# Performance work log

Measured on AMD Instinct MI355X. Metric: run time of the kernel, lower is better.

Reference implementation:

```python
import jax, jax.numpy as jnp
import numpy as np

N_NODES = 50000
N_EDGES = 800000
IN_FEATS = 128
HIDDEN = 128
OUT_LEN = 128


def setup_inputs() -> dict:
    key = jax.random.key(0)
    ks = jax.random.split(key, 8)
    feat = jax.random.normal(ks[0], (N_NODES, IN_FEATS), dtype=jnp.float32)
    # Glorot-ish init for weights, zeros for bias (DGL GraphConv default)
    def w(k, fi, fo):
        return jax.random.normal(k, (fi, fo), dtype=jnp.float32) / np.sqrt(fi)
    W1 = w(ks[1], IN_FEATS, HIDDEN)
    W2 = w(ks[2], HIDDEN, HIDDEN)
    W3 = w(ks[3], HIDDEN, OUT_LEN)
    b1 = jnp.zeros((HIDDEN,), jnp.float32)
    b2 = jnp.zeros((HIDDEN,), jnp.float32)
    b3 = jnp.zeros((OUT_LEN,), jnp.float32)
    src = jax.random.randint(ks[4], (N_EDGES,), 0, N_NODES, dtype=jnp.int32)
    dst = jax.random.randint(ks[5], (N_EDGES,), 0, N_NODES, dtype=jnp.int32)
    return {"feat": feat, "W1": W1, "b1": b1, "W2": W2, "b2": b2,
            "W3": W3, "b3": b3, "src": src, "dst": dst}


def _degree_norm(idx, n):
    # degree counts, clamped to min 1 (DGL behavior), then ^{-1/2}
    deg = jax.ops.segment_sum(jnp.ones_like(idx, dtype=jnp.float32), idx,
                              num_segments=n)
    return jax.lax.rsqrt(jnp.maximum(deg, 1.0))


def _graph_conv(x, W, b, src, dst, out_norm, in_norm):
    # DGL GraphConv, norm='both':
    # h = D_dst^{-1/2} * segsum_dst( D_src^{-1/2} * x[src] ) @ W + b
    h = x * out_norm[:, None]
    m = jax.ops.segment_sum(h[src], dst, num_segments=x.shape[0])  # [N, d]
    m = m * in_norm[:, None]
    return m @ W + b


def reference(feat, W1, b1, W2, b2, W3, b3, src, dst):
    out_norm = _degree_norm(src, feat.shape[0])  # out-degree norm (source)
    in_norm = _degree_norm(dst, feat.shape[0])   # in-degree norm (dest)
    h = jax.nn.relu(_graph_conv(feat, W1, b1, src, dst, out_norm, in_norm))
    h = jax.nn.relu(_graph_conv(h, W2, b2, src, dst, out_norm, in_norm))
    h = _graph_conv(h, W3, b3, src, dst, out_norm, in_norm)
    # single graph: mean_nodes == mean over all nodes, then squeeze -> [out_len]
    return jnp.mean(h, axis=0)
```

## Files before the change

### kernel.cpp

```cpp
#include <hip/hip_runtime.h>

#define N_NODES 50000
#define N_EDGES 800000
#define F 128
#define SCAN_NB 49
#define CH 64
#define EPC (N_EDGES / CH)
#define HALF 25000
#define QTR 12500
#define BSTRIDE 17
#define AGG_NB (N_NODES / 4)
#define GB ((N_NODES + 63) / 64)

typedef __bf16 bf16x8 __attribute__((ext_vector_type(8)));
typedef float  f32x4  __attribute__((ext_vector_type(4)));
typedef float  f32x2  __attribute__((ext_vector_type(2)));

__device__ inline unsigned short f2bf(float f) {
    unsigned u = __float_as_uint(f);
    u += 0x7FFF + ((u >> 16) & 1);
    return (unsigned short)(u >> 16);
}
__device__ inline unsigned packbf2(float a, float b) {
    return (unsigned)f2bf(a) | ((unsigned)f2bf(b) << 16);
}

__device__ inline void fp8x8_to_f32(uint2 u, float* f) {
    f32x2 v0 = __builtin_amdgcn_cvt_pk_f32_fp8(u.x, false);
    f32x2 v1 = __builtin_amdgcn_cvt_pk_f32_fp8(u.x, true);
    f32x2 v2 = __builtin_amdgcn_cvt_pk_f32_fp8(u.y, false);
    f32x2 v3 = __builtin_amdgcn_cvt_pk_f32_fp8(u.y, true);
    f[0] = v0.x; f[1] = v0.y; f[2] = v1.x; f[3] = v1.y;
    f[4] = v2.x; f[5] = v2.y; f[6] = v3.x; f[7] = v3.y;
}
__device__ inline unsigned f32x4_to_fp8(float a, float b, float c, float d) {
    unsigned r = __builtin_amdgcn_cvt_pk_fp8_f32(a, b, 0, false);
    r = __builtin_amdgcn_cvt_pk_fp8_f32(c, d, r, true);
    return r;
}

__global__ __launch_bounds__(1024) void hist_kernel(const int* __restrict__ src,
                                                    const int* __restrict__ dst,
                                                    unsigned char* __restrict__ Hs8,
                                                    unsigned char* __restrict__ Hd8,
                                                    int* __restrict__ bsump) {
    __shared__ unsigned hist[HALF / 4];
    int bx = blockIdx.x;
    int c = bx >> 2, t = bx & 1, h = (bx >> 1) & 1;
    const int* ids = t ? dst : src;
    unsigned char* H = t ? Hd8 : Hs8;
    int base = h * HALF;
    for (int j = threadIdx.x; j < HALF / 4; j += 1024) hist[j] = 0;
    __syncthreads();
    const int4* ids4 = (const int4*)(ids + c * EPC);
    for (int i = threadIdx.x; i < EPC / 4; i += 1024) {
        int4 v = ids4[i];
#pragma unroll
        for (int k = 0; k < 4; k++) {
            int id = ((k == 0) ? v.x : (k == 1) ? v.y : (k == 2) ? v.z : v.w) - base;
            if ((unsigned)id < (unsigned)HALF)
                atomicAdd(&hist[id >> 2], 1u << ((id & 3) * 8));
        }
    }
    __syncthreads();
    unsigned* Hw = (unsigned*)(H + (size_t)c * N_NODES + base);
    for (int j = threadIdx.x; j < HALF / 4; j += 1024) Hw[j] = hist[j];
    if (t) {
        int w = threadIdx.x >> 6, lane = threadIdx.x & 63;
        for (int r = w; r < SCAN_NB; r += 16) {
            int gi0 = max(r * 1024, base);
            int gi1 = min(r * 1024 + 1024, base + HALF);
            int s = 0;
            for (int li = gi0 - base + lane; li < gi1 - base; li += 64)
                s += (hist[li >> 2] >> ((li & 3) * 8)) & 255;
#pragma unroll
            for (int off = 32; off; off >>= 1) s += __shfl_down(s, off);
            if (lane == 0) bsump[(c * 2 + h) * SCAN_NB + r] = s;
        }
    }
}

__global__ __launch_bounds__(1024) void scanC_kernel(const unsigned char* __restrict__ Hs8,
                                                     const unsigned char* __restrict__ Hd8,
                                                     const int* __restrict__ bsump,
                                                     float* __restrict__ onorm,
                                                     float* __restrict__ inorm,
                                                     int* __restrict__ rowst,
                                                     unsigned char* __restrict__ P8) {
    __shared__ int wsum[16];
    __shared__ int tot[SCAN_NB];
    int t = threadIdx.x, lane = t & 63, w = t >> 6;
    int i = blockIdx.x * 1024 + t;
    if (t < SCAN_NB) {
        int s = 0;
        for (int p = 0; p < 2 * CH; p++) s += bsump[p * SCAN_NB + t];
        tot[t] = s;
    }
    int dd = 0;
    if (i < N_NODES) {
        int ds = 0, run = 0;
        for (int c = 0; c < CH; c++) {
            size_t o = (size_t)c * N_NODES + i;
            ds += Hs8[o];
            P8[o] = (unsigned char)run;
            run += Hd8[o];
        }
        dd = run;
        onorm[i] = rsqrtf(fmaxf((float)ds, 1.0f));
        inorm[i] = rsqrtf(fmaxf((float)dd, 1.0f));
    }
    int v = dd, incl = v;
#pragma unroll
    for (int off = 1; off < 64; off <<= 1) {
        int u = __shfl_up(incl, off);
        if (lane >= off) incl += u;
    }
    if (lane == 63) wsum[w] = incl;
    __syncthreads();
    if (t == 0) {
        int s = 0;
        for (int r = 0; r < (int)blockIdx.x; r++) s += tot[r];
#pragma unroll
        for (int k = 0; k < 16; k++) { int x = wsum[k]; wsum[k] = s; s += x; }
    }
    __syncthreads();
    incl += wsum[w];
    if (i < N_NODES) {
        rowst[i] = incl - v;
        if (i == N_NODES - 1) rowst[N_NODES] = incl;
    }
}

__global__ __launch_bounds__(1024) void tqsc_kernel(const int* __restrict__ src,
                                                    const int* __restrict__ dst,
                                                    const float* __restrict__ inorm,
                                                    float* __restrict__ Tq,
                                                    const int* __restrict__ rowst,
                                                    const unsigned char* __restrict__ P8,
                                                    int* __restrict__ esrc,
                                                    const float* __restrict__ feat,
                                                    const float* __restrict__ onorm,
                                                    uint2* __restrict__ xq,
                                                    const float* __restrict__ W1,
                                                    const float* __restrict__ W2,
                                                    unsigned short* __restrict__ Wt) {
    __shared__ float a[QTR];
    __shared__ int cur[QTR];
    int bx = blockIdx.x;
    int c = bx >> 2, q = bx & 3;
    int base = q * QTR;

    for (int j = threadIdx.x; j < QTR; j += 1024) {
        a[j] = 0.0f;
        cur[j] = rowst[base + j] + (int)P8[(size_t)c * N_NODES + base + j];
    }
    __syncthreads();

    const int4* src4 = (const int4*)(src + c * EPC);
    const int4* dst4 = (const int4*)(dst + c * EPC);
    for (int i = threadIdx.x; i < EPC / 4; i += 1024) {
        int4 s4 = src4[i], d4 = dst4[i];
#pragma unroll
        for (int k = 0; k < 4; k++) {
            int s = (k == 0) ? s4.x : (k == 1) ? s4.y : (k == 2) ? s4.z : s4.w;
            int d = (k == 0) ? d4.x : (k == 1) ? d4.y : (k == 2) ? d4.z : d4.w;
            int sq = s - base;
            if ((unsigned)sq < (unsigned)QTR)
                atomicAdd(&a[sq], inorm[d]);
            int dq = d - base;
            if ((unsigned)dq < (unsigned)QTR) {
                int pos = atomicAdd(&cur[dq], 1);
                esrc[pos] = s;
            }
        }
    }
    __syncthreads();
    for (int j = threadIdx.x; j < QTR; j += 1024)
        Tq[(size_t)c * N_NODES + base + j] = a[j];

    int T = gridDim.x * 1024;
    int id0 = bx * 1024 + threadIdx.x;
    for (int i = id0; i < N_NODES * F / 8; i += T) {
        float w = onorm[i >> 4];
        const float4* xv = (const float4*)feat;
        float4 v0 = xv[i * 2], v1 = xv[i * 2 + 1];
        uint2 o;
        o.x = f32x4_to_fp8(v0.x * w, v0.y * w, v0.z * w, v0.w * w);
        o.y = f32x4_to_fp8(v1.x * w, v1.y * w, v1.z * w, v1.w * w);
        xq[i] = o;
    }
    for (int i = id0; i < 2 * F * F; i += T) {
        int wi = i >> 14, rem = i & 16383;
        int n = rem >> 7, k = rem & 127;
        const float* W = wi ? W2 : W1;
        Wt[(size_t)wi * F * F + (size_t)n * F + k] = f2bf(W[k * F + n]);
    }
}

template <int QT>
__global__ __launch_bounds__(256) void agg_csr_kernel(const uint2* __restrict__ xq,
                                                      uint4* __restrict__ mb,
                                                      const int* __restrict__ rowst,
                                                      const int* __restrict__ esrc,
                                                      const float* __restrict__ inorm,
                                                      const float* __restrict__ Tq,
                                                      float* __restrict__ qt) {
    int w = threadIdx.x >> 6;
    int lane = threadIdx.x & 63;
    int g = lane >> 4, t = lane & 15;
    int row = blockIdx.x * 4 + w;
    int beg = __builtin_amdgcn_readfirstlane(rowst[row]);
    int end = __builtin_amdgcn_readfirstlane(rowst[row + 1]);
    float acc[8];
#pragma unroll
    for (int k = 0; k < 8; k++) acc[k] = 0.0f;

    for (int e = beg; e < end; e += 16) {
        int ea = min(e + g,      end - 1);
        int eb = min(e + 4 + g,  end - 1);
        int ec = min(e + 8 + g,  end - 1);
        int ed = min(e + 12 + g, end - 1);
        int sa = esrc[ea], sb = esrc[eb], sc = esrc[ec], sd = esrc[ed];
        uint2 ua = xq[(size_t)sa * 16 + t];
        uint2 ub = xq[(size_t)sb * 16 + t];
        uint2 uc = xq[(size_t)sc * 16 + t];
        uint2 ud = xq[(size_t)sd * 16 + t];
        float wa = (e + g      < end) ? 1.0f : 0.0f;
        float wb = (e + 4 + g  < end) ? 1.0f : 0.0f;
        float wc = (e + 8 + g  < end) ? 1.0f : 0.0f;
        float wd = (e + 12 + g < end) ? 1.0f : 0.0f;
        float fa[8], fb[8], fc[8], fd[8];
        fp8x8_to_f32(ua, fa); fp8x8_to_f32(ub, fb);
        fp8x8_to_f32(uc, fc); fp8x8_to_f32(ud, fd);
#pragma unroll
        for (int k = 0; k < 8; k++)
            acc[k] += fa[k] * wa + fb[k] * wb + fc[k] * wc + fd[k] * wd;
    }
#pragma unroll
    for (int k = 0; k < 8; k++) {
        acc[k] += __shfl_xor(acc[k], 16, 64);
        acc[k] += __shfl_xor(acc[k], 32, 64);
    }
    if (g == 0) {
        float inw = inorm[row];
        uint4 o;
        o.x = packbf2(acc[0] * inw, acc[1] * inw);
        o.y = packbf2(acc[2] * inw, acc[3] * inw);
        o.z = packbf2(acc[4] * inw, acc[5] * inw);
        o.w = packbf2(acc[6] * inw, acc[7] * inw);
        mb[(size_t)row * 16 + t] = o;
    }
    if (QT) {
        int i = blockIdx.x * 256 + threadIdx.x;
        if (i < N_NODES) {
            float s = 0.0f;
            for (int c = 0; c < CH; c++) s += Tq[(size_t)c * N_NODES + i];
            qt[i] = s;
        }
    }
}

template <int FINAL>
__global__ __launch_bounds__(256) void mfma_gemm_kernel(const unsigned short* __restrict__ A,
                                                        const unsigned short* __restrict__ Wt,
                                                        const float* __restrict__ bias,
                                                        const float* __restrict__ onorm,
                                                        unsigned char* __restrict__ Y8,
                                                        const float* __restrict__ qt,
                                                        float* __restrict__ part2) {
    __shared__ uint4 sB[F * BSTRIDE];
    __shared__ float sPf[4][F];
    int tid = threadIdx.x;
    int w = tid >> 6;
    int lane = tid & 63;
    int quad = lane >> 4, r16 = lane & 15;
    int row0 = blockIdx.x * 64 + w * 16;

    int arow = min(row0 + r16, N_NODES - 1);
    const uint4* Arow = (const uint4*)(A + (size_t)arow * F);
    uint4 a[4];
#pragma unroll
    for (int kk = 0; kk < 4; kk++) a[kk] = Arow[kk * 4 + quad];

    const uint4* G = (const uint4*)Wt;
    for (int j = tid; j < F * 16; j += 256)
        sB[(j >> 4) * BSTRIDE + (j & 15)] = G[j];

    f32x4 acc[8];
#pragma unroll
    for (int t = 0; t < 8; t++) acc[t] = (f32x4){0.f, 0.f, 0.f, 0.f};
    __syncthreads();

#pragma unroll
    for (int kk = 0; kk < 4; kk++) {
        bf16x8 av = __builtin_bit_cast(bf16x8, a[kk]);
#pragma unroll
        for (int t = 0; t < 8; t++) {
            bf16x8 bv = __builtin_bit_cast(bf16x8,
                sB[(t * 16 + r16) * BSTRIDE + kk * 4 + quad]);
            acc[t] = __builtin_amdgcn_mfma_f32_16x16x32_bf16(av, bv, acc[t], 0, 0, 0);
        }
    }

    float rw[4];
#pragma unroll
    for (int reg = 0; reg < 4; reg++) {
        int row = row0 + quad * 4 + reg;
        rw[reg] = (row < N_NODES) ? (FINAL ? qt[row] * onorm[row] : onorm[row]) : 0.0f;
    }

    if (!FINAL) {
#pragma unroll
        for (int t = 0; t < 8; t++) {
            int col = t * 16 + r16;
            float bb = bias[col];
#pragma unroll
            for (int reg = 0; reg < 4; reg++) {
                int row = row0 + quad * 4 + reg;
                if (row < N_NODES) {
                    float v = fmaxf(acc[t][reg] + bb, 0.0f) * rw[reg];
                    unsigned p = __builtin_amdgcn_cvt_pk_fp8_f32(v, v, 0, false);
                    Y8[(size_t)row * F + col] = (unsigned char)(p & 0xFF);
                }
            }
        }
    } else {
#pragma unroll
        for (int t = 0; t < 8; t++) {
            int col = t * 16 + r16;
            float bb = bias[col];
            float p = 0.0f;
#pragma unroll
            for (int reg = 0; reg < 4; reg++)
                p += fmaxf(acc[t][reg] + bb, 0.0f) * rw[reg];
            p += __shfl_xor(p, 16, 64);
            p += __shfl_xor(p, 32, 64);
            if (quad == 0) sPf[w][col] = p;
        }
        __syncthreads();
        if (tid < F)
            part2[(size_t)blockIdx.x * F + tid] =
                sPf[0][tid] + sPf[1][tid] + sPf[2][tid] + sPf[3][tid];
    }
}

__global__ __launch_bounds__(1024) void final_kernel(const float* __restrict__ part2,
                                                     const float* __restrict__ W3,
                                                     const float* __restrict__ b3,
                                                     float* __restrict__ out) {
    __shared__ float sc[8][F];
    int tid = threadIdx.x;
    int col = tid & 127, sl = tid >> 7;
    float acc = 0.0f;
    for (int b = sl; b < GB; b += 8) acc += part2[(size_t)b * F + col];
    sc[sl][col] = acc;
    __syncthreads();
    if (tid < F) {
        float s = 0.0f;
#pragma unroll
        for (int k = 0; k < 8; k++) s += sc[k][tid];
        sc[0][tid] = s * (1.0f / (float)N_NODES);
    }
    __syncthreads();
    if (tid < F) {
        float o = b3[tid];
        for (int k = 0; k < F; k++) o += sc[0][k] * W3[k * F + tid];
        out[tid] = o;
    }
}

extern "C" void kernel_launch(void* const* d_in, const int* in_sizes, int n_in,
                              void* d_out, int out_size, void* d_ws, size_t ws_size,
                              hipStream_t stream) {
    const float* feat = (const float*)d_in[0];
    const float* W1   = (const float*)d_in[1];
    const float* b1   = (const float*)d_in[2];
    const float* W2   = (const float*)d_in[3];
    const float* b2   = (const float*)d_in[4];
    const float* W3   = (const float*)d_in[5];
    const float* b3   = (const float*)d_in[6];
    const int*   src  = (const int*)d_in[7];
    const int*   dst  = (const int*)d_in[8];
    float* out = (float*)d_out;

    char* ws = (char*)d_ws;
    size_t off = 0;
    uint4* mb    = (uint4*)(ws + off); off += (size_t)N_NODES * F * 2;
    float* Tq    = (float*)(ws + off); off += (size_t)CH * N_NODES * 4;
    uint2* xq    = (uint2*)(ws + off); off += (size_t)N_NODES * F;
    uint2* hq    = (uint2*)(ws + off); off += (size_t)N_NODES * F;
    unsigned char* Hs8 = (unsigned char*)(ws + off); off += (size_t)CH * N_NODES;
    unsigned char* Hd8 = (unsigned char*)(ws + off); off += (size_t)CH * N_NODES;
    unsigned char* P8  = (unsigned char*)(ws + off); off += (size_t)CH * N_NODES;
    int*   esrc  = (int*)  (ws + off); off += (size_t)N_EDGES * 4;
    unsigned short* Wt = (unsigned short*)(ws + off); off += 2 * F * F * 2;
    float* part2 = (float*)(ws + off); off += (size_t)GB * F * 4;
    float* onorm = (float*)(ws + off); off += N_NODES * 4;
    float* inorm = (float*)(ws + off); off += N_NODES * 4;
    float* qt    = (float*)(ws + off); off += N_NODES * 4;
    int*   rowst = (int*)  (ws + off); off += (N_NODES + 1) * 4;
    int*   bsump = (int*)  (ws + off); off += 2 * CH * SCAN_NB * 4;

    hist_kernel<<<4 * CH, 1024, 0, stream>>>(src, dst, Hs8, Hd8, bsump);
    scanC_kernel<<<SCAN_NB, 1024, 0, stream>>>(Hs8, Hd8, bsump, onorm, inorm,
                                               rowst, P8);
    tqsc_kernel<<<4 * CH, 1024, 0, stream>>>(src, dst, inorm, Tq, rowst, P8,
                                             esrc, feat, onorm, xq, W1, W2, Wt);

    agg_csr_kernel<1><<<AGG_NB, 256, 0, stream>>>(xq, mb, rowst, esrc, inorm, Tq, qt);
    mfma_gemm_kernel<0><<<GB, 256, 0, stream>>>((const unsigned short*)mb, Wt, b1,
                                                onorm, (unsigned char*)hq, qt, part2);
    agg_csr_kernel<0><<<AGG_NB, 256, 0, stream>>>(hq, mb, rowst, esrc, inorm, Tq, qt);
    mfma_gemm_kernel<1><<<GB, 256, 0, stream>>>((const unsigned short*)mb, Wt + F * F,
                                                b2, onorm, (unsigned char*)hq, qt, part2);
    final_kernel<<<1, 1024, 0, stream>>>(part2, W3, b3, out);
}
```

Measured before the change: 212.4 us.

## Split histogram into quarters and widen degree scan to 196 small blocks

After: 224.1 us. 1.05x slower.

```diff
diff --git a/kernel.cpp b/kernel.cpp
--- a/kernel.cpp
+++ b/kernel.cpp
@@ -3,10 +3,9 @@
 #define N_NODES 50000
 #define N_EDGES 800000
 #define F 128
-#define SCAN_NB 49
+#define RNG 196
 #define CH 64
 #define EPC (N_EDGES / CH)
-#define HALF 25000
 #define QTR 12500
 #define BSTRIDE 17
 #define AGG_NB (N_NODES / 4)
@@ -44,13 +43,13 @@
                                                     unsigned char* __restrict__ Hs8,
                                                     unsigned char* __restrict__ Hd8,
                                                     int* __restrict__ bsump) {
-    __shared__ unsigned hist[HALF / 4];
+    __shared__ unsigned hist[QTR / 4];
     int bx = blockIdx.x;
-    int c = bx >> 2, t = bx & 1, h = (bx >> 1) & 1;
+    int c = bx >> 3, t = bx & 1, h = (bx >> 1) & 3;
     const int* ids = t ? dst : src;
     unsigned char* H = t ? Hd8 : Hs8;
-    int base = h * HALF;
-    for (int j = threadIdx.x; j < HALF / 4; j += 1024) hist[j] = 0;
+    int base = h * QTR;
+    for (int j = threadIdx.x; j < QTR / 4; j += 1024) hist[j] = 0;
     __syncthreads();
     const int4* ids4 = (const int4*)(ids + c * EPC);
     for (int i = threadIdx.x; i < EPC / 4; i += 1024) {
@@ -58,44 +57,41 @@
 #pragma unroll
         for (int k = 0; k < 4; k++) {
             int id = ((k == 0) ? v.x : (k == 1) ? v.y : (k == 2) ? v.z : v.w) - base;
-            if ((unsigned)id < (unsigned)HALF)
+            if ((unsigned)id < (unsigned)QTR)
                 atomicAdd(&hist[id >> 2], 1u << ((id & 3) * 8));
         }
     }
     __syncthreads();
     unsigned* Hw = (unsigned*)(H + (size_t)c * N_NODES + base);
-    for (int j = threadIdx.x; j < HALF / 4; j += 1024) Hw[j] = hist[j];
+    for (int j = threadIdx.x; j < QTR / 4; j += 1024) Hw[j] = hist[j];
     if (t) {
         int w = threadIdx.x >> 6, lane = threadIdx.x & 63;
-        for (int r = w; r < SCAN_NB; r += 16) {
-            int gi0 = max(r * 1024, base);
-            int gi1 = min(r * 1024 + 1024, base + HALF);
+        for (int r = w; r < RNG; r += 16) {
+            int gi0 = max(r * 256, base);
+            int gi1 = min(r * 256 + 256, base + QTR);
             int s = 0;
             for (int li = gi0 - base + lane; li < gi1 - base; li += 64)
                 s += (hist[li >> 2] >> ((li & 3) * 8)) & 255;
 #pragma unroll
             for (int off = 32; off; off >>= 1) s += __shfl_down(s, off);
-            if (lane == 0) bsump[(c * 2 + h) * SCAN_NB + r] = s;
-        }
-    }
-}
-
-__global__ __launch_bounds__(1024) void scanC_kernel(const unsigned char* __restrict__ Hs8,
-                                                     const unsigned char* __restrict__ Hd8,
-                                                     const int* __restrict__ bsump,
-                                                     float* __restrict__ onorm,
-                                                     float* __restrict__ inorm,
-                                                     int* __restrict__ rowst,
-                                                     unsigned char* __restrict__ P8) {
-    __shared__ int wsum[16];
-    __shared__ int tot[SCAN_NB];
+            if (lane == 0) bsump[(c * 4 + h) * RNG + r] = s;
+        }
+    }
+}
+
+__global__ __launch_bounds__(256) void scanC_kernel(const unsigned char* __restrict__ Hs8,
+                                                    const unsigned char* __restrict__ Hd8,
+                                                    const int* __restrict__ bsump,
+                                                    float* __restrict__ onorm,
+                                                    float* __restrict__ inorm,
+                                                    int* __restrict__ rowst,
+                                                    unsigned char* __restrict__ P8) {
+    __shared__ int wsum[4];
+    __shared__ int sbase;
     int t = threadIdx.x, lane = t & 63, w = t >> 6;
-    int i = blockIdx.x * 1024 + t;
-    if (t < SCAN_NB) {
-        int s = 0;
-        for (int p = 0; p < 2 * CH; p++) s += bsump[p * SCAN_NB + t];
-        tot[t] = s;
-    }
+    int b = blockIdx.x;
+    int i = b * 256 + t;
+    if (t == 0) sbase = 0;
     int dd = 0;
     if (i < N_NODES) {
         int ds = 0, run = 0;
@@ -116,12 +112,21 @@
         if (lane >= off) incl += u;
     }
     if (lane == 63) wsum[w] = incl;
+    int bs = 0;
+    for (int r = t; r < b; r += 256) {
+        int s = 0;
+        for (int p = 0; p < 4 * CH; p++) s += bsump[p * RNG + r];
+        bs += s;
+    }
+#pragma unroll
+    for (int off = 32; off; off >>= 1) bs += __shfl_down(bs, off);
+    __syncthreads();
+    if (lane == 0 && bs != 0) atomicAdd(&sbase, bs);
     __syncthreads();
     if (t == 0) {
-        int s = 0;
-        for (int r = 0; r < (int)blockIdx.x; r++) s += tot[r];
-#pragma unroll
-        for (int k = 0; k < 16; k++) { int x = wsum[k]; wsum[k] = s; s += x; }
+        int s = sbase;
+#pragma unroll
+        for (int k = 0; k < 4; k++) { int x = wsum[k]; wsum[k] = s; s += x; }
     }
     __syncthreads();
     incl += wsum[w];
@@ -144,15 +149,19 @@
                                                     const float* __restrict__ W1,
                                                     const float* __restrict__ W2,
                                                     unsigned short* __restrict__ Wt) {
-    __shared__ float a[QTR];
-    __shared__ int cur[QTR];
+    __shared__ __align__(16) float a[QTR];
+    __shared__ __align__(16) int cur[QTR];
     int bx = blockIdx.x;
     int c = bx >> 2, q = bx & 3;
     int base = q * QTR;
 
-    for (int j = threadIdx.x; j < QTR; j += 1024) {
-        a[j] = 0.0f;
-        cur[j] = rowst[base + j] + (int)P8[(size_t)c * N_NODES + base + j];
+    for (int j = 4 * threadIdx.x; j < QTR; j += 4096) {
+        *(float4*)&a[j] = (float4){0.f, 0.f, 0.f, 0.f};
+        int4 rs = *(const int4*)&rowst[base + j];
+        uchar4 p = *(const uchar4*)&P8[(size_t)c * N_NODES + base + j];
+        int4 cv;
+        cv.x = rs.x + p.x; cv.y = rs.y + p.y; cv.z = rs.z + p.z; cv.w = rs.w + p.w;
+        *(int4*)&cur[j] = cv;
     }
     __syncthreads();
 
@@ -175,8 +184,8 @@
         }
     }
     __syncthreads();
-    for (int j = threadIdx.x; j < QTR; j += 1024)
-        Tq[(size_t)c * N_NODES + base + j] = a[j];
+    for (int j = 4 * threadIdx.x; j < QTR; j += 4096)
+        *(float4*)&Tq[(size_t)c * N_NODES + base + j] = *(const float4*)&a[j];
 
     int T = gridDim.x * 1024;
     int id0 = bx * 1024 + threadIdx.x;
@@ -399,11 +408,11 @@
     float* inorm = (float*)(ws + off); off += N_NODES * 4;
     float* qt    = (float*)(ws + off); off += N_NODES * 4;
     int*   rowst = (int*)  (ws + off); off += (N_NODES + 1) * 4;
-    int*   bsump = (int*)  (ws + off); off += 2 * CH * SCAN_NB * 4;
-
-    hist_kernel<<<4 * CH, 1024, 0, stream>>>(src, dst, Hs8, Hd8, bsump);
-    scanC_kernel<<<SCAN_NB, 1024, 0, stream>>>(Hs8, Hd8, bsump, onorm, inorm,
-                                               rowst, P8);
+    int*   bsump = (int*)  (ws + off); off += 4 * CH * RNG * 4;
+
+    hist_kernel<<<8 * CH, 1024, 0, stream>>>(src, dst, Hs8, Hd8, bsump);
+    scanC_kernel<<<RNG, 256, 0, stream>>>(Hs8, Hd8, bsump, onorm, inorm,
+                                          rowst, P8);
     tqsc_kernel<<<4 * CH, 1024, 0, stream>>>(src, dst, inorm, Tq, rowst, P8,
                                              esrc, feat, onorm, xq, W1, W2, Wt);
 
```
